# Kernel optimization log

Measured on AMD Instinct MI355X. Metric: run time of the kernel, lower is better.

The kernel has to match this reference:

```python
import jax, jax.numpy as jnp
import numpy as np

B, D = 90000, 100
E_GNN, E_MLP = 4, 4
E = E_GNN + E_MLP + 1  # 9
K = 2
NOISE_EPS = 0.01
LOSS_COEF = 0.4
GATE_MEAN, GATE_STD = 0.1, 1.0  # registered buffers in the torch module


def setup_inputs() -> dict:
    key = jax.random.key(0)
    ks = jax.random.split(key, 16)
    f = jax.random.normal
    return {
        "memory_feats": f(ks[0], (B, D), jnp.float32),
        "recent_raw": f(ks[1], (B, E_MLP, D), jnp.float32),
        "spatial_raw": f(ks[2], (B, E_GNN, D), jnp.float32),
        "node_feats_src": f(ks[3], (B, D), jnp.float32),
        "noise": f(ks[4], (B, E), jnp.float32),
        "deg_coef": f(ks[5], (1, D, 2), jnp.float32),
        "w_gate": f(ks[6], (6 * D, E), jnp.float32) * 0.05,
        "w_noise": f(ks[7], (6 * D, E), jnp.float32) * 0.05,
        "src_w": f(ks[8], (D, D), jnp.float32) * 0.1,
        "src_b": f(ks[9], (D,), jnp.float32) * 0.1,
        "dst_w": f(ks[10], (D, D), jnp.float32) * 0.1,
        "dst_b": f(ks[11], (D,), jnp.float32) * 0.1,
        "out_w": f(ks[12], (D, 1), jnp.float32) * 0.1,
        "out_b": f(ks[13], (1,), jnp.float32) * 0.1,
        "degree": jax.random.randint(ks[14], (B,), 0, 64, jnp.int32),
        "neg_samples": 1,
    }


def _cv_squared(x):
    # torch .var() is unbiased (ddof=1)
    return jnp.var(x, ddof=1) / (jnp.mean(x) ** 2 + 1e-10)


def _norm_cdf(v):
    return jax.scipy.stats.norm.cdf(v, loc=GATE_MEAN, scale=GATE_STD)


def reference(memory_feats, recent_raw, spatial_raw, node_feats_src, noise,
              deg_coef, w_gate, w_noise, src_w, src_b, dst_w, dst_b,
              out_w, out_b, degree, neg_samples):
    # memory expert output (dropout is identity in eval; relu applied)
    mem = jax.nn.relu(memory_feats)                        # [B, D]
    rec = jax.nn.relu(recent_raw)                          # [B, Em, D]
    log_deg = jnp.log(degree.astype(mem.dtype) + 1.0)      # [B]
    # degree-conditioned reweighting: stack([r, r*log_deg],-1) * deg_coef, sum(-1)
    c0, c1 = deg_coef[0, :, 0], deg_coef[0, :, 1]          # [D]
    spa = spatial_raw * (c0 + log_deg[:, None, None] * c1)  # [B, Eg, D]

    combine = jnp.concatenate([mem[:, None, :], spa, rec], axis=1)  # [B, E, D]
    result_spa = spa.mean(axis=1)
    result_rec = rec.mean(axis=1)
    x1 = mem + result_spa + result_rec
    x2 = mem * result_spa * result_rec
    cat = jnp.concatenate([mem, result_spa, result_rec, x1, x2, node_feats_src], axis=1)  # [B, 6D]

    # noisy top-k gating (train=True)
    clean = cat @ w_gate                                   # [B, E]
    std = jax.nn.softplus(cat @ w_noise) + NOISE_EPS
    noisy = clean + noise * std
    top_vals, top_idx = jax.lax.top_k(noisy, K + 1)        # [B, K+1]
    topk_gates = jax.nn.softmax(top_vals[:, :K], axis=1)
    b_idx = jnp.arange(noisy.shape[0])[:, None]
    gates = jnp.zeros_like(noisy).at[b_idx, top_idx[:, :K]].set(topk_gates)

    # prob of being in top-k for load-balance loss
    thr_in = top_vals[:, K][:, None]
    thr_out = top_vals[:, K - 1][:, None]
    is_in = noisy > thr_in
    prob = jnp.where(is_in,
                     _norm_cdf((clean - thr_in) / std),
                     _norm_cdf((clean - thr_out) / std))
    load = prob.sum(axis=0)
    importance = gates.sum(axis=0)
    loss = LOSS_COEF * (_cv_squared(importance) + _cv_squared(load))

    out = jnp.einsum('bed,be->bd', combine, gates)         # [B, D]

    # edge predictor
    num_edge = out.shape[0] // (neg_samples + 2)
    h_src = out[:num_edge] @ src_w + src_b
    h_pos = out[num_edge:2 * num_edge] @ dst_w + dst_b
    h_neg = out[2 * num_edge:] @ dst_w + dst_b
    pos = jax.nn.relu(h_src + h_pos) @ out_w + out_b       # [num_edge, 1]
    neg = jax.nn.relu(jnp.tile(h_src, (neg_samples, 1)) + h_neg) @ out_w + out_b
    return pos, neg, loss
```

## Files before the change

### kernel.cpp

```cpp
#include <hip/hip_runtime.h>
#include <math.h>

#define DD 100

#define DPP_ADD(v, ctrl) ((v) + __int_as_float(__builtin_amdgcn_update_dpp( \
    0, __float_as_int(v), (ctrl), 0xf, 0xf, true)))

__device__ __forceinline__ float blo(unsigned u){
  union { unsigned i; float f; } c; c.i = u << 16; return c.f;
}
__device__ __forceinline__ float bhi(unsigned u){
  union { unsigned i; float f; } c; c.i = u & 0xFFFF0000u; return c.f;
}
__device__ __forceinline__ unsigned short f2bf(float f){
  unsigned u = __float_as_uint(f);
  unsigned r = (u + 0x7FFFu + ((u >> 16) & 1u)) >> 16;
  return (unsigned short)r;
}
__device__ __forceinline__ float phi_fast(float z){
  float x  = z * 0.70710678118654752440f;
  float ax = fabsf(x);
  float t  = __builtin_amdgcn_rcpf(1.0f + 0.3275911f*ax);
  float p  = t*(0.254829592f + t*(-0.284496736f + t*(1.421413741f
           + t*(-1.453152027f + t*1.061405429f))));
  float e  = __expf(-ax*ax);
  float erfv = copysignf(1.0f - p*e, x);
  return 0.5f*(1.0f + erfv);
}
__device__ __forceinline__ float4 relu4(float4 v){
  return make_float4(fmaxf(v.x,0.f), fmaxf(v.y,0.f), fmaxf(v.z,0.f), fmaxf(v.w,0.f));
}
#define GETJ4(v,j) ((j==0)?(v).x:(j==1)?(v).y:(j==2)?(v).z:(v).w)

__global__ void k_fold(const float* __restrict__ wg, const float* __restrict__ wn,
                       float* __restrict__ wfold)
{
  int idx = blockIdx.x*256 + threadIdx.x;
  if (idx >= 9000) return;
  int dim = idx/90, r = idx%90, s = r/18, e = r%18;
  const float* W = (e < 9) ? wg : wn;
  int ee = (e < 9) ? e : e-9;
  int rowA = (s==0) ? dim : (s==1) ? 100+dim : (s==2) ? 200+dim
           : (s==3) ? 400+dim : 500+dim;
  float v = W[rowA*9 + ee] + ((s < 3) ? W[(300+dim)*9 + ee] : 0.f);
  wfold[idx] = v;
}

__global__ __launch_bounds__(256) void k_gate(
    const float* __restrict__ memf, const float* __restrict__ recr,
    const float* __restrict__ spar, const float* __restrict__ nsrc,
    const float* __restrict__ noise, const float* __restrict__ degc,
    const float* __restrict__ wfold, const int* __restrict__ degree,
    float4* __restrict__ gateinfo, float* __restrict__ partials, int B)
{
  __shared__ __align__(16) float sWF[100*92];
  __shared__ __align__(16) float sC0[DD], sC1[DD];
  __shared__ float sPart[4][18];

  for (int i = threadIdx.x; i < 9000; i += 256){
    int d = i/90, r = i%90;
    int slot = (d>>2) + 25*(d&3);
    sWF[slot*92 + r] = wfold[i];
  }
  for (int i = threadIdx.x; i < DD; i += 256){ sC0[i]=degc[2*i]; sC1[i]=degc[2*i+1]; }
  __syncthreads();

  const int wave = threadIdx.x >> 6, lane = threadIdx.x & 63;
  const int fq = lane & 3, rl = lane >> 2;
  const float4* sC04 = (const float4*)sC0;
  const float4* sC14 = (const float4*)sC1;

  float ldA[9], imA[9];
  #pragma unroll
  for (int e = 0; e < 9; e++){ ldA[e]=0.f; imA[e]=0.f; }

  const int rA = blockIdx.x*128 + wave*32 + rl*2;
  const int rB = rA + 1;
  const bool vA = rA < B, vB = rB < B;
  const int rcA = vA ? rA : B-1, rcB = vB ? rB : B-1;
  const float ldgA = __logf((float)degree[rcA] + 1.0f);
  const float ldgB = __logf((float)degree[rcB] + 1.0f);

  const float* pmA = memf + (size_t)rcA*DD;  const float* pmB = memf + (size_t)rcB*DD;
  const float* psA = spar + (size_t)rcA*4*DD;const float* psB = spar + (size_t)rcB*4*DD;
  const float* prA = recr + (size_t)rcA*4*DD;const float* prB = recr + (size_t)rcB*4*DD;
  const float* pnA = nsrc + (size_t)rcA*DD;  const float* pnB = nsrc + (size_t)rcB*DD;

  float cgA[9], cnA[9], cgB[9], cnB[9];
  #pragma unroll
  for (int e = 0; e < 9; e++){ cgA[e]=0.f; cnA[e]=0.f; cgB[e]=0.f; cnB[e]=0.f; }

  for (int k = 0; k < 7; k++){
    const int c = fq + 4*k;
    const float fz = (c < 25) ? 1.f : 0.f;
    const int ce = (c < 25) ? c : 0;
    const float4 c04 = sC04[ce], c14 = sC14[ce];

    float4 dA0, dA1, dA2, dA3, dA4;
    {
      float4 me = *(const float4*)(pmA + 4*ce);
      float4 s0 = *(const float4*)(psA + 0*DD + 4*ce);
      float4 s1 = *(const float4*)(psA + 1*DD + 4*ce);
      float4 s2 = *(const float4*)(psA + 2*DD + 4*ce);
      float4 s3 = *(const float4*)(psA + 3*DD + 4*ce);
      float4 r0 = *(const float4*)(prA + 0*DD + 4*ce);
      float4 r1 = *(const float4*)(prA + 1*DD + 4*ce);
      float4 r2 = *(const float4*)(prA + 2*DD + 4*ce);
      float4 r3 = *(const float4*)(prA + 3*DD + 4*ce);
      float4 nv = *(const float4*)(pnA + 4*ce);
      float4 m4 = relu4(me);
      float4 sc = make_float4(c04.x + ldgA*c14.x, c04.y + ldgA*c14.y,
                              c04.z + ldgA*c14.z, c04.w + ldgA*c14.w);
      float4 rs4 = make_float4((s0.x+s1.x+s2.x+s3.x)*0.25f*sc.x,
                               (s0.y+s1.y+s2.y+s3.y)*0.25f*sc.y,
                               (s0.z+s1.z+s2.z+s3.z)*0.25f*sc.z,
                               (s0.w+s1.w+s2.w+s3.w)*0.25f*sc.w);
      float4 a0 = relu4(r0), a1 = relu4(r1), a2 = relu4(r2), a3 = relu4(r3);
      float4 rr4 = make_float4((a0.x+a1.x+a2.x+a3.x)*0.25f,
                               (a0.y+a1.y+a2.y+a3.y)*0.25f,
                               (a0.z+a1.z+a2.z+a3.z)*0.25f,
                               (a0.w+a1.w+a2.w+a3.w)*0.25f);
      dA0 = make_float4(m4.x*fz, m4.y*fz, m4.z*fz, m4.w*fz);
      dA1 = make_float4(rs4.x*fz, rs4.y*fz, rs4.z*fz, rs4.w*fz);
      dA2 = make_float4(rr4.x*fz, rr4.y*fz, rr4.z*fz, rr4.w*fz);
      dA4 = make_float4(nv.x*fz, nv.y*fz, nv.z*fz, nv.w*fz);
      dA3 = make_float4(dA0.x*dA1.x*dA2.x, dA0.y*dA1.y*dA2.y,
                        dA0.z*dA1.z*dA2.z, dA0.w*dA1.w*dA2.w);
    }
    float4 dB0, dB1, dB2, dB3, dB4;
    {
      float4 me = *(const float4*)(pmB + 4*ce);
      float4 s0 = *(const float4*)(psB + 0*DD + 4*ce);
      float4 s1 = *(const float4*)(psB + 1*DD + 4*ce);
      float4 s2 = *(const float4*)(psB + 2*DD + 4*ce);
      float4 s3 = *(const float4*)(psB + 3*DD + 4*ce);
      float4 r0 = *(const float4*)(prB + 0*DD + 4*ce);
      float4 r1 = *(const float4*)(prB + 1*DD + 4*ce);
      float4 r2 = *(const float4*)(prB + 2*DD + 4*ce);
      float4 r3 = *(const float4*)(prB + 3*DD + 4*ce);
      float4 nv = *(const float4*)(pnB + 4*ce);
      float4 m4 = relu4(me);
      float4 sc = make_float4(c04.x + ldgB*c14.x, c04.y + ldgB*c14.y,
                              c04.z + ldgB*c14.z, c04.w + ldgB*c14.w);
      float4 rs4 = make_float4((s0.x+s1.x+s2.x+s3.x)*0.25f*sc.x,
                               (s0.y+s1.y+s2.y+s3.y)*0.25f*sc.y,
                               (s0.z+s1.z+s2.z+s3.z)*0.25f*sc.z,
                               (s0.w+s1.w+s2.w+s3.w)*0.25f*sc.w);
      float4 a0 = relu4(r0), a1 = relu4(r1), a2 = relu4(r2), a3 = relu4(r3);
      float4 rr4 = make_float4((a0.x+a1.x+a2.x+a3.x)*0.25f,
                               (a0.y+a1.y+a2.y+a3.y)*0.25f,
                               (a0.z+a1.z+a2.z+a3.z)*0.25f,
                               (a0.w+a1.w+a2.w+a3.w)*0.25f);
      dB0 = make_float4(m4.x*fz, m4.y*fz, m4.z*fz, m4.w*fz);
      dB1 = make_float4(rs4.x*fz, rs4.y*fz, rs4.z*fz, rs4.w*fz);
      dB2 = make_float4(rr4.x*fz, rr4.y*fz, rr4.z*fz, rr4.w*fz);
      dB4 = make_float4(nv.x*fz, nv.y*fz, nv.z*fz, nv.w*fz);
      dB3 = make_float4(dB0.x*dB1.x*dB2.x, dB0.y*dB1.y*dB2.y,
                        dB0.z*dB1.z*dB2.z, dB0.w*dB1.w*dB2.w);
    }

    #pragma unroll
    for (int j = 0; j < 4; j++){
      const float a0 = GETJ4(dA0,j), a1 = GETJ4(dA1,j), a2 = GETJ4(dA2,j);
      const float a3 = GETJ4(dA3,j), a4 = GETJ4(dA4,j);
      const float b0 = GETJ4(dB0,j), b1 = GETJ4(dB1,j), b2 = GETJ4(dB2,j);
      const float b3 = GETJ4(dB3,j), b4 = GETJ4(dB4,j);
      const float4* wpj = (const float4*)(sWF + (ce + 25*j)*92);
      #pragma unroll
      for (int tq = 0; tq < 23; tq++){
        float4 w = wpj[tq];
        #pragma unroll
        for (int u = 0; u < 4; u++){
          const int ww = 4*tq + u;
          if (ww < 90){
            const int seg = ww/18, e = ww%18;
            float wv = (u==0)?w.x:(u==1)?w.y:(u==2)?w.z:w.w;
            float dA = (seg==0)?a0:(seg==1)?a1:(seg==2)?a2:(seg==3)?a3:a4;
            float dB = (seg==0)?b0:(seg==1)?b1:(seg==2)?b2:(seg==3)?b3:b4;
            if (e < 9){ cgA[e] += dA*wv; cgB[e] += dB*wv; }
            else      { cnA[e-9] += dA*wv; cnB[e-9] += dB*wv; }
          }
        }
      }
    }
  }

  #pragma unroll
  for (int e = 0; e < 9; e++){
    cgA[e] = DPP_ADD(cgA[e], 0xB1); cgA[e] = DPP_ADD(cgA[e], 0x4E);
    cnA[e] = DPP_ADD(cnA[e], 0xB1); cnA[e] = DPP_ADD(cnA[e], 0x4E);
    cgB[e] = DPP_ADD(cgB[e], 0xB1); cgB[e] = DPP_ADD(cgB[e], 0x4E);
    cnB[e] = DPP_ADD(cnB[e], 0xB1); cnB[e] = DPP_ADD(cnB[e], 0x4E);
  }

  const bool selB = (fq >= 2);
  const int rowS = selB ? rB : rA;
  const bool vS = rowS < B;
  const int rcS = vS ? rowS : B-1;
  float fg[9], fn[9];
  #pragma unroll
  for (int e = 0; e < 9; e++){
    fg[e] = selB ? cgB[e] : cgA[e];
    fn[e] = selB ? cnB[e] : cnA[e];
  }

  float sdv[9], rsd[9], nz[9];
  #pragma unroll
  for (int e = 0; e < 9; e++){
    float x = fn[e];
    float spl = fmaxf(x, 0.f) + __logf(1.0f + __expf(-fabsf(x)));
    sdv[e] = spl + 0.01f;
    rsd[e] = __builtin_amdgcn_rcpf(sdv[e]);
    nz[e]  = fg[e] + noise[(size_t)rcS*9 + e] * sdv[e];
  }
  float v1 = -3.402823e38f, v2 = v1, v3 = v1; int i1 = -1, i2 = -1;
  #pragma unroll
  for (int e = 0; e < 9; e++){
    float v = nz[e];
    if (v > v1){ v3=v2; v2=v1; i2=i1; v1=v; i1=e; }
    else if (v > v2){ v3=v2; v2=v; i2=e; }
    else if (v > v3){ v3=v; }
  }
  float tt = __expf(v2 - v1);
  float g1 = __builtin_amdgcn_rcpf(1.0f + tt);
  float g2 = tt*g1;

  float ld[9], im[9];
  #pragma unroll
  for (int e = 0; e < 9; e++){
    float thr = (nz[e] > v3) ? v3 : v2;
    float z = (fg[e] - thr)*rsd[e] - 0.1f;
    ld[e] = vS ? phi_fast(z) : 0.f;
    im[e] = vS ? ((e==i1) ? g1 : ((e==i2) ? g2 : 0.f)) : 0.f;
  }
  if ((fq & 1) == 0 && vS)
    gateinfo[rowS] = make_float4(g1, g2, __int_as_float(i1), __int_as_float(i2));

  #pragma unroll
  for (int e = 0; e < 9; e++){
    #pragma unroll
    for (int off = 4; off < 64; off <<= 1){
      ld[e] += __shfl_xor(ld[e], off, 64);
      im[e] += __shfl_xor(im[e], off, 64);
    }
    ld[e] += __shfl_xor(ld[e], 2, 64);
    im[e] += __shfl_xor(im[e], 2, 64);
  }
  if (lane == 0){
    #pragma unroll
    for (int e = 0; e < 9; e++){ sPart[wave][e] = im[e]; sPart[wave][9+e] = ld[e]; }
  }
  __syncthreads();
  if (threadIdx.x < 18){
    float s = sPart[0][threadIdx.x] + sPart[1][threadIdx.x]
            + sPart[2][threadIdx.x] + sPart[3][threadIdx.x];
    partials[blockIdx.x*18 + threadIdx.x] = s;
  }
}

__global__ __launch_bounds__(256) void k_mix(
    const float* __restrict__ memf, const float* __restrict__ recr,
    const float* __restrict__ spar, const float* __restrict__ degc,
    const int* __restrict__ degree, const float4* __restrict__ gateinfo,
    float* __restrict__ outm, int B)
{
  const int total = B*25;
  for (int idx = blockIdx.x*256 + threadIdx.x; idx < total; idx += gridDim.x*256){
    int row = idx / 25, q = idx - row*25;
    float4 gi = gateinfo[row];
    float gv[2] = {gi.x, gi.y};
    int   ei[2] = {__float_as_int(gi.z), __float_as_int(gi.w)};
    float4 acc = make_float4(0.f,0.f,0.f,0.f);
    #pragma unroll
    for (int s = 0; s < 2; s++){
      int e = ei[s]; float g = gv[s];
      float4 v;
      if (e == 0){
        v = relu4(*(const float4*)(memf + (size_t)row*DD + 4*q));
      } else if (e < 5){
        float ldg = __logf((float)degree[row] + 1.0f);
        float4 ca = *(const float4*)(degc + 8*q);
        float4 cb = *(const float4*)(degc + 8*q + 4);
        float4 sv = *(const float4*)(spar + ((size_t)row*4 + (e-1))*DD + 4*q);
        v = make_float4(sv.x*(ca.x + ldg*ca.y), sv.y*(ca.z + ldg*ca.w),
                        sv.z*(cb.x + ldg*cb.y), sv.w*(cb.z + ldg*cb.w));
      } else {
        v = relu4(*(const float4*)(recr + ((size_t)row*4 + (e-5))*DD + 4*q));
      }
      acc.x += g*v.x; acc.y += g*v.y; acc.z += g*v.z; acc.w += g*v.w;
    }
    ((float4*)outm)[(size_t)row*25 + q] = acc;
  }
}

__global__ __launch_bounds__(1024) void k_loss(const float* __restrict__ partials,
                                               int nblk, float* __restrict__ dloss)
{
  __shared__ float sS[18][57];
  int t = threadIdx.x;
  if (t < 1008){
    int k = t % 18, c = t / 18;
    float s = 0.f;
    for (int b = c; b < nblk; b += 56) s += partials[b*18 + k];
    sS[k][c] = s;
  }
  __syncthreads();
  if (t < 18){
    float tot = 0.f;
    #pragma unroll
    for (int c = 0; c < 56; c++) tot += sS[t][c];
    sS[t][56] = tot;
  }
  __syncthreads();
  if (t == 0){
    float mi = 0.f, ml = 0.f;
    #pragma unroll
    for (int e = 0; e < 9; e++){ mi += sS[e][56]; ml += sS[9+e][56]; }
    mi *= (1.f/9.f); ml *= (1.f/9.f);
    float vi = 0.f, vl = 0.f;
    #pragma unroll
    for (int e = 0; e < 9; e++){
      float a = sS[e][56]   - mi; vi += a*a;
      float b = sS[9+e][56] - ml; vl += b*b;
    }
    vi *= (1.f/8.f); vl *= (1.f/8.f);
    *dloss = 0.4f * (vi/(mi*mi + 1e-10f) + vl/(ml*ml + 1e-10f));
  }
}

__global__ __launch_bounds__(512) void k_edge(
    const float* __restrict__ om,
    const float* __restrict__ sw, const float* __restrict__ sb,
    const float* __restrict__ dw, const float* __restrict__ db,
    const float* __restrict__ ow, const float* __restrict__ ob,
    float* __restrict__ dout, int NE)
{
  __shared__ __align__(4) unsigned short sSW[DD*102];
  __shared__ __align__(4) unsigned short sDW[DD*102];
  __shared__ float sSB[DD], sDB[DD], sOW[DD];

  for (int i = threadIdx.x; i < DD*DD; i += 512){
    int k = i / DD, d = i % DD;
    sSW[d*102 + k] = f2bf(sw[i]);
    sDW[d*102 + k] = f2bf(dw[i]);
  }
  for (int i = threadIdx.x; i < DD; i += 512){ sSB[i]=sb[i]; sDB[i]=db[i]; sOW[i]=ow[i]; }
  __syncthreads();

  const int wave = threadIdx.x >> 6, lane = threadIdx.x & 63;
  const int grp = blockIdx.x*8 + wave;
  const int e0 = grp*4;
  if (e0 >= NE) return;
  const int e0u = __builtin_amdgcn_readfirstlane(e0);
  const float* oS = om + (size_t)e0u*DD;
  const float* oP = om + ((size_t)(NE  + e0u))*DD;
  const float* oN = om + ((size_t)(2*NE + e0u))*DD;
  const int d0 = lane, d1 = lane + 64;
  const bool h1 = (d1 < DD);
  const int dc1 = h1 ? d1 : 0;

  float aS[4][2], aP[4][2], aN[4][2];
  #pragma unroll
  for (int r = 0; r < 4; r++){
    aS[r][0]=0.f; aS[r][1]=0.f; aP[r][0]=0.f; aP[r][1]=0.f; aN[r][0]=0.f; aN[r][1]=0.f;
  }

  for (int k = 0; k < DD; k += 4){
    unsigned uA = *(const unsigned*)&sSW[d0 *102 + k];
    unsigned uB = *(const unsigned*)&sSW[d0 *102 + k + 2];
    unsigned uC = *(const unsigned*)&sSW[dc1*102 + k];
    unsigned uD = *(const unsigned*)&sSW[dc1*102 + k + 2];
    unsigned uE = *(const unsigned*)&sDW[d0 *102 + k];
    unsigned uF = *(const unsigned*)&sDW[d0 *102 + k + 2];
    unsigned uG = *(const unsigned*)&sDW[dc1*102 + k];
    unsigned uH = *(const unsigned*)&sDW[dc1*102 + k + 2];
    float wS00=blo(uA), wS01=bhi(uA), wS02=blo(uB), wS03=bhi(uB);
    float wS10=blo(uC), wS11=bhi(uC), wS12=blo(uD), wS13=bhi(uD);
    float wD00=blo(uE), wD01=bhi(uE), wD02=blo(uF), wD03=bhi(uF);
    float wD10=blo(uG), wD11=bhi(uG), wD12=blo(uH), wD13=bhi(uH);
    #pragma unroll
    for (int r = 0; r < 4; r++){
      float4 ov = *(const float4*)(oS + r*DD + k);
      float4 pv = *(const float4*)(oP + r*DD + k);
      float4 nv = *(const float4*)(oN + r*DD + k);
      aS[r][0] += ov.x*wS00 + ov.y*wS01 + ov.z*wS02 + ov.w*wS03;
      aS[r][1] += ov.x*wS10 + ov.y*wS11 + ov.z*wS12 + ov.w*wS13;
      aP[r][0] += pv.x*wD00 + pv.y*wD01 + pv.z*wD02 + pv.w*wD03;
      aP[r][1] += pv.x*wD10 + pv.y*wD11 + pv.z*wD12 + pv.w*wD13;
      aN[r][0] += nv.x*wD00 + nv.y*wD01 + nv.z*wD02 + nv.w*wD03;
      aN[r][1] += nv.x*wD10 + nv.y*wD11 + nv.z*wD12 + nv.w*wD13;
    }
  }

  float owa = sOW[d0], owb = sOW[dc1];
  float sba = sSB[d0], sbb = sSB[dc1];
  float dba = sDB[d0], dbb = sDB[dc1];
  float ob0 = ob[0];
  #pragma unroll
  for (int r = 0; r < 4; r++){
    float hs0 = aS[r][0] + sba, hp0 = aP[r][0] + dba, hn0 = aN[r][0] + dba;
    float tp = fmaxf(hs0 + hp0, 0.f)*owa;
    float tn = fmaxf(hs0 + hn0, 0.f)*owa;
    if (h1){
      float hs1 = aS[r][1] + sbb, hp1 = aP[r][1] + dbb, hn1 = aN[r][1] + dbb;
      tp += fmaxf(hs1 + hp1, 0.f)*owb;
      tn += fmaxf(hs1 + hn1, 0.f)*owb;
    }
    #pragma unroll
    for (int off = 32; off > 0; off >>= 1){
      tp += __shfl_xor(tp, off, 64);
      tn += __shfl_xor(tn, off, 64);
    }
    if (lane == 0){
      dout[e0 + r]      = tp + ob0;
      dout[NE + e0 + r] = tn + ob0;
    }
  }
}

extern "C" void kernel_launch(void* const* d_in, const int* in_sizes, int n_in,
                              void* d_out, int out_size, void* d_ws, size_t ws_size,
                              hipStream_t stream)
{
  (void)n_in; (void)out_size; (void)ws_size;
  const float* memf  = (const float*)d_in[0];
  const float* recr  = (const float*)d_in[1];
  const float* spar  = (const float*)d_in[2];
  const float* nsrc  = (const float*)d_in[3];
  const float* noise = (const float*)d_in[4];
  const float* degc  = (const float*)d_in[5];
  const float* wg    = (const float*)d_in[6];
  const float* wn    = (const float*)d_in[7];
  const float* sw    = (const float*)d_in[8];
  const float* sb    = (const float*)d_in[9];
  const float* dw    = (const float*)d_in[10];
  const float* db    = (const float*)d_in[11];
  const float* ow    = (const float*)d_in[12];
  const float* ob    = (const float*)d_in[13];
  const int*   deg   = (const int*)d_in[14];

  const int B  = in_sizes[0] / DD;
  const int NE = B / 3;
  const int blocksA = (B + 127) / 128;

  float4* gateinfo = (float4*)d_ws;
  float*  outm     = (float*)(gateinfo + B);
  float*  partials = outm + (size_t)B*DD;
  float*  wfold    = partials + (size_t)blocksA*18;
  float*  dout     = (float*)d_out;

  k_fold<<<dim3(36), dim3(256), 0, stream>>>(wg, wn, wfold);
  k_gate<<<dim3(blocksA), dim3(256), 0, stream>>>(memf, recr, spar, nsrc, noise,
                                                  degc, wfold, deg, gateinfo,
                                                  partials, B);
  k_mix<<<dim3(2048), dim3(256), 0, stream>>>(memf, recr, spar, degc, deg,
                                              gateinfo, outm, B);
  k_loss<<<dim3(1), dim3(1024), 0, stream>>>(partials, blocksA, dout + 2*NE);
  const int blocks2 = (NE/4 + 7) / 8;
  k_edge<<<dim3(blocks2), dim3(512), 0, stream>>>(outm, sw, sb, dw, db, ow, ob, dout, NE);
}
```

Measured before the change: 264.5 us.

## Split gate GEMV work across lanes by dimension parity and gate/noise half

```diff
diff --git a/kernel.cpp b/kernel.cpp
--- a/kernel.cpp
+++ b/kernel.cpp
@@ -30,51 +30,41 @@
 __device__ __forceinline__ float4 relu4(float4 v){
   return make_float4(fmaxf(v.x,0.f), fmaxf(v.y,0.f), fmaxf(v.z,0.f), fmaxf(v.w,0.f));
 }
-#define GETJ4(v,j) ((j==0)?(v).x:(j==1)?(v).y:(j==2)?(v).z:(v).w)
 
 __global__ void k_fold(const float* __restrict__ wg, const float* __restrict__ wn,
-                       float* __restrict__ wfold)
+                       float* __restrict__ wfold2)
 {
   int idx = blockIdx.x*256 + threadIdx.x;
   if (idx >= 9000) return;
-  int dim = idx/90, r = idx%90, s = r/18, e = r%18;
-  const float* W = (e < 9) ? wg : wn;
-  int ee = (e < 9) ? e : e-9;
+  int dim = idx/90, r = idx%90, eh = r/45, i = r%45, s = i/9, e = i%9;
+  const float* W = eh ? wn : wg;
   int rowA = (s==0) ? dim : (s==1) ? 100+dim : (s==2) ? 200+dim
            : (s==3) ? 400+dim : 500+dim;
-  float v = W[rowA*9 + ee] + ((s < 3) ? W[(300+dim)*9 + ee] : 0.f);
-  wfold[idx] = v;
+  float v = W[rowA*9 + e] + ((s < 3) ? W[(300+dim)*9 + e] : 0.f);
+  wfold2[(dim*2 + eh)*52 + i] = v;
 }
 
 __global__ __launch_bounds__(256) void k_gate(
     const float* __restrict__ memf, const float* __restrict__ recr,
     const float* __restrict__ spar, const float* __restrict__ nsrc,
     const float* __restrict__ noise, const float* __restrict__ degc,
-    const float* __restrict__ wfold, const int* __restrict__ degree,
+    const float* __restrict__ wfold2, const int* __restrict__ degree,
     float4* __restrict__ gateinfo, float* __restrict__ partials, int B)
 {
-  __shared__ __align__(16) float sWF[100*92];
-  __shared__ __align__(16) float sC0[DD], sC1[DD];
+  __shared__ __align__(16) float sW2[200*52];
+  __shared__ __align__(8) float2 sCC[DD];
   __shared__ float sPart[4][18];
 
-  for (int i = threadIdx.x; i < 9000; i += 256){
-    int d = i/90, r = i%90;
-    int slot = (d>>2) + 25*(d&3);
-    sWF[slot*92 + r] = wfold[i];
-  }
-  for (int i = threadIdx.x; i < DD; i += 256){ sC0[i]=degc[2*i]; sC1[i]=degc[2*i+1]; }
+  for (int i = threadIdx.x; i < 10400; i += 256) sW2[i] = wfold2[i];
+  for (int i = threadIdx.x; i < DD; i += 256)
+    sCC[i] = make_float2(degc[2*i], degc[2*i+1]);
   __syncthreads();
 
   const int wave = threadIdx.x >> 6, lane = threadIdx.x & 63;
-  const int fq = lane & 3, rl = lane >> 2;
-  const float4* sC04 = (const float4*)sC0;
-  const float4* sC14 = (const float4*)sC1;
-
-  float ldA[9], imA[9];
-  #pragma unroll
-  for (int e = 0; e < 9; e++){ ldA[e]=0.f; imA[e]=0.f; }
-
-  const int rA = blockIdx.x*128 + wave*32 + rl*2;
+  const int fq = lane & 3, grp = lane >> 2;
+  const int dp = fq & 1, eh = fq >> 1;
+
+  const int rA = blockIdx.x*128 + wave*32 + grp*2;
   const int rB = rA + 1;
   const bool vA = rA < B, vB = rB < B;
   const int rcA = vA ? rA : B-1, rcB = vB ? rB : B-1;
@@ -86,111 +76,92 @@
   const float* prA = recr + (size_t)rcA*4*DD;const float* prB = recr + (size_t)rcB*4*DD;
   const float* pnA = nsrc + (size_t)rcA*DD;  const float* pnB = nsrc + (size_t)rcB*DD;
 
-  float cgA[9], cnA[9], cgB[9], cnB[9];
-  #pragma unroll
-  for (int e = 0; e < 9; e++){ cgA[e]=0.f; cnA[e]=0.f; cgB[e]=0.f; cnB[e]=0.f; }
-
-  for (int k = 0; k < 7; k++){
-    const int c = fq + 4*k;
-    const float fz = (c < 25) ? 1.f : 0.f;
-    const int ce = (c < 25) ? c : 0;
-    const float4 c04 = sC04[ce], c14 = sC14[ce];
-
-    float4 dA0, dA1, dA2, dA3, dA4;
+  float accA[9], accB[9];
+  #pragma unroll
+  for (int e = 0; e < 9; e++){ accA[e]=0.f; accB[e]=0.f; }
+
+  for (int k = 0; k < 50; k++){
+    const int d2 = 2*k;
+    const int dim = d2 + dp;
+    const float2 cc = sCC[dim];
+
+    float fA0, fA1, fA2, fA3, fA4;
     {
-      float4 me = *(const float4*)(pmA + 4*ce);
-      float4 s0 = *(const float4*)(psA + 0*DD + 4*ce);
-      float4 s1 = *(const float4*)(psA + 1*DD + 4*ce);
-      float4 s2 = *(const float4*)(psA + 2*DD + 4*ce);
-      float4 s3 = *(const float4*)(psA + 3*DD + 4*ce);
-      float4 r0 = *(const float4*)(prA + 0*DD + 4*ce);
-      float4 r1 = *(const float4*)(prA + 1*DD + 4*ce);
-      float4 r2 = *(const float4*)(prA + 2*DD + 4*ce);
-      float4 r3 = *(const float4*)(prA + 3*DD + 4*ce);
-      float4 nv = *(const float4*)(pnA + 4*ce);
-      float4 m4 = relu4(me);
-      float4 sc = make_float4(c04.x + ldgA*c14.x, c04.y + ldgA*c14.y,
-                              c04.z + ldgA*c14.z, c04.w + ldgA*c14.w);
-      float4 rs4 = make_float4((s0.x+s1.x+s2.x+s3.x)*0.25f*sc.x,
-                               (s0.y+s1.y+s2.y+s3.y)*0.25f*sc.y,
-                               (s0.z+s1.z+s2.z+s3.z)*0.25f*sc.z,
-                               (s0.w+s1.w+s2.w+s3.w)*0.25f*sc.w);
-      float4 a0 = relu4(r0), a1 = relu4(r1), a2 = relu4(r2), a3 = relu4(r3);
-      float4 rr4 = make_float4((a0.x+a1.x+a2.x+a3.x)*0.25f,
-                               (a0.y+a1.y+a2.y+a3.y)*0.25f,
-                               (a0.z+a1.z+a2.z+a3.z)*0.25f,
-                               (a0.w+a1.w+a2.w+a3.w)*0.25f);
-      dA0 = make_float4(m4.x*fz, m4.y*fz, m4.z*fz, m4.w*fz);
-      dA1 = make_float4(rs4.x*fz, rs4.y*fz, rs4.z*fz, rs4.w*fz);
-      dA2 = make_float4(rr4.x*fz, rr4.y*fz, rr4.z*fz, rr4.w*fz);
-      dA4 = make_float4(nv.x*fz, nv.y*fz, nv.z*fz, nv.w*fz);
-      dA3 = make_float4(dA0.x*dA1.x*dA2.x, dA0.y*dA1.y*dA2.y,
-                        dA0.z*dA1.z*dA2.z, dA0.w*dA1.w*dA2.w);
-    }
-    float4 dB0, dB1, dB2, dB3, dB4;
+      float2 me = *(const float2*)(pmA + d2);
+      float2 s0 = *(const float2*)(psA + 0*DD + d2);
+      float2 s1 = *(const float2*)(psA + 1*DD + d2);
+      float2 s2 = *(const float2*)(psA + 2*DD + d2);
+      float2 s3 = *(const float2*)(psA + 3*DD + d2);
+      float2 r0 = *(const float2*)(prA + 0*DD + d2);
+      float2 r1 = *(const float2*)(prA + 1*DD + d2);
+      float2 r2 = *(const float2*)(prA + 2*DD + d2);
+      float2 r3 = *(const float2*)(prA + 3*DD + d2);
+      float2 nv = *(const float2*)(pnA + d2);
+      float mm = fmaxf(dp ? me.y : me.x, 0.f);
+      float sa = (dp ? s0.y : s0.x) + (dp ? s1.y : s1.x)
+               + (dp ? s2.y : s2.x) + (dp ? s3.y : s3.x);
+      float rr = fmaxf(dp ? r0.y : r0.x, 0.f) + fmaxf(dp ? r1.y : r1.x, 0.f)
+               + fmaxf(dp ? r2.y : r2.x, 0.f) + fmaxf(dp ? r3.y : r3.x, 0.f);
+      fA0 = mm;
+      fA1 = sa*0.25f*(cc.x + ldgA*cc.y);
+      fA2 = rr*0.25f;
+      fA3 = fA0*fA1*fA2;
+      fA4 = dp ? nv.y : nv.x;
+    }
+    float fB0, fB1, fB2, fB3, fB4;
     {
-      float4 me = *(const float4*)(pmB + 4*ce);
-      float4 s0 = *(const float4*)(psB + 0*DD + 4*ce);
-      float4 s1 = *(const float4*)(psB + 1*DD + 4*ce);
-      float4 s2 = *(const float4*)(psB + 2*DD + 4*ce);
-      float4 s3 = *(const float4*)(psB + 3*DD + 4*ce);
-      float4 r0 = *(const float4*)(prB + 0*DD + 4*ce);
-      float4 r1 = *(const float4*)(prB + 1*DD + 4*ce);
-      float4 r2 = *(const float4*)(prB + 2*DD + 4*ce);
-      float4 r3 = *(const float4*)(prB + 3*DD + 4*ce);
-      float4 nv = *(const float4*)(pnB + 4*ce);
-      float4 m4 = relu4(me);
-      float4 sc = make_float4(c04.x + ldgB*c14.x, c04.y + ldgB*c14.y,
-                              c04.z + ldgB*c14.z, c04.w + ldgB*c14.w);
-      float4 rs4 = make_float4((s0.x+s1.x+s2.x+s3.x)*0.25f*sc.x,
-                               (s0.y+s1.y+s2.y+s3.y)*0.25f*sc.y,
-                               (s0.z+s1.z+s2.z+s3.z)*0.25f*sc.z,
-                               (s0.w+s1.w+s2.w+s3.w)*0.25f*sc.w);
-      float4 a0 = relu4(r0), a1 = relu4(r1), a2 = relu4(r2), a3 = relu4(r3);
-      float4 rr4 = make_float4((a0.x+a1.x+a2.x+a3.x)*0.25f,
-                               (a0.y+a1.y+a2.y+a3.y)*0.25f,
-                               (a0.z+a1.z+a2.z+a3.z)*0.25f,
-                               (a0.w+a1.w+a2.w+a3.w)*0.25f);
-      dB0 = make_float4(m4.x*fz, m4.y*fz, m4.z*fz, m4.w*fz);
-      dB1 = make_float4(rs4.x*fz, rs4.y*fz, rs4.z*fz, rs4.w*fz);
-      dB2 = make_float4(rr4.x*fz, rr4.y*fz, rr4.z*fz, rr4.w*fz);
-      dB4 = make_float4(nv.x*fz, nv.y*fz, nv.z*fz, nv.w*fz);
-      dB3 = make_float4(dB0.x*dB1.x*dB2.x, dB0.y*dB1.y*dB2.y,
-                        dB0.z*dB1.z*dB2.z, dB0.w*dB1.w*dB2.w);
-    }
-
-    #pragma unroll
-    for (int j = 0; j < 4; j++){
-      const float a0 = GETJ4(dA0,j), a1 = GETJ4(dA1,j), a2 = GETJ4(dA2,j);
-      const float a3 = GETJ4(dA3,j), a4 = GETJ4(dA4,j);
-      const float b0 = GETJ4(dB0,j), b1 = GETJ4(dB1,j), b2 = GETJ4(dB2,j);
-      const float b3 = GETJ4(dB3,j), b4 = GETJ4(dB4,j);
-      const float4* wpj = (const float4*)(sWF + (ce + 25*j)*92);
+      float2 me = *(const float2*)(pmB + d2);
+      float2 s0 = *(const float2*)(psB + 0*DD + d2);
+      float2 s1 = *(const float2*)(psB + 1*DD + d2);
+      float2 s2 = *(const float2*)(psB + 2*DD + d2);
+      float2 s3 = *(const float2*)(psB + 3*DD + d2);
+      float2 r0 = *(const float2*)(prB + 0*DD + d2);
+      float2 r1 = *(const float2*)(prB + 1*DD + d2);
+      float2 r2 = *(const float2*)(prB + 2*DD + d2);
+      float2 r3 = *(const float2*)(prB + 3*DD + d2);
+      float2 nv = *(const float2*)(pnB + d2);
+      float mm = fmaxf(dp ? me.y : me.x, 0.f);
+      float sa = (dp ? s0.y : s0.x) + (dp ? s1.y : s1.x)
+               + (dp ? s2.y : s2.x) + (dp ? s3.y : s3.x);
+      float rr = fmaxf(dp ? r0.y : r0.x, 0.f) + fmaxf(dp ? r1.y : r1.x, 0.f)
+               + fmaxf(dp ? r2.y : r2.x, 0.f) + fmaxf(dp ? r3.y : r3.x, 0.f);
+      fB0 = mm;
+      fB1 = sa*0.25f*(cc.x + ldgB*cc.y);
+      fB2 = rr*0.25f;
+      fB3 = fB0*fB1*fB2;
+      fB4 = dp ? nv.y : nv.x;
+    }
+
+    const float4* wp = (const float4*)(sW2 + (size_t)(dim*2 + eh)*52);
+    #pragma unroll
+    for (int tq = 0; tq < 12; tq++){
+      float4 w = wp[tq];
       #pragma unroll
-      for (int tq = 0; tq < 23; tq++){
-        float4 w = wpj[tq];
-        #pragma unroll
-        for (int u = 0; u < 4; u++){
-          const int ww = 4*tq + u;
-          if (ww < 90){
-            const int seg = ww/18, e = ww%18;
-            float wv = (u==0)?w.x:(u==1)?w.y:(u==2)?w.z:w.w;
-            float dA = (seg==0)?a0:(seg==1)?a1:(seg==2)?a2:(seg==3)?a3:a4;
-            float dB = (seg==0)?b0:(seg==1)?b1:(seg==2)?b2:(seg==3)?b3:b4;
-            if (e < 9){ cgA[e] += dA*wv; cgB[e] += dB*wv; }
-            else      { cnA[e-9] += dA*wv; cnB[e-9] += dB*wv; }
-          }
+      for (int u = 0; u < 4; u++){
+        const int i = 4*tq + u;
+        if (i < 45){
+          const int s = i/9, e = i%9;
+          float wv = (u==0)?w.x:(u==1)?w.y:(u==2)?w.z:w.w;
+          float dA = (s==0)?fA0:(s==1)?fA1:(s==2)?fA2:(s==3)?fA3:fA4;
+          float dB = (s==0)?fB0:(s==1)?fB1:(s==2)?fB2:(s==3)?fB3:fB4;
+          accA[e] += dA*wv;
+          accB[e] += dB*wv;
         }
       }
     }
   }
 
-  #pragma unroll
-  for (int e = 0; e < 9; e++){
-    cgA[e] = DPP_ADD(cgA[e], 0xB1); cgA[e] = DPP_ADD(cgA[e], 0x4E);
-    cnA[e] = DPP_ADD(cnA[e], 0xB1); cnA[e] = DPP_ADD(cnA[e], 0x4E);
-    cgB[e] = DPP_ADD(cgB[e], 0xB1); cgB[e] = DPP_ADD(cgB[e], 0x4E);
-    cnB[e] = DPP_ADD(cnB[e], 0xB1); cnB[e] = DPP_ADD(cnB[e], 0x4E);
+  float cgA[9], cnA[9], cgB[9], cnB[9];
+  #pragma unroll
+  for (int e = 0; e < 9; e++){
+    float sA = DPP_ADD(accA[e], 0xB1);
+    float oA = __shfl_xor(sA, 2, 64);
+    cgA[e] = eh ? oA : sA;
+    cnA[e] = eh ? sA : oA;
+    float sB = DPP_ADD(accB[e], 0xB1);
+    float oB = __shfl_xor(sB, 2, 64);
+    cgB[e] = eh ? oB : sB;
+    cnB[e] = eh ? sB : oB;
   }
 
   const bool selB = (fq >= 2);
@@ -446,12 +417,12 @@
   float4* gateinfo = (float4*)d_ws;
   float*  outm     = (float*)(gateinfo + B);
   float*  partials = outm + (size_t)B*DD;
-  float*  wfold    = partials + (size_t)blocksA*18;
+  float*  wfold2   = partials + (size_t)blocksA*18;
   float*  dout     = (float*)d_out;
 
-  k_fold<<<dim3(36), dim3(256), 0, stream>>>(wg, wn, wfold);
+  k_fold<<<dim3(36), dim3(256), 0, stream>>>(wg, wn, wfold2);
   k_gate<<<dim3(blocksA), dim3(256), 0, stream>>>(memf, recr, spar, nsrc, noise,
-                                                  degc, wfold, deg, gateinfo,
+                                                  degc, wfold2, deg, gateinfo,
                                                   partials, B);
   k_mix<<<dim3(2048), dim3(256), 0, stream>>>(memf, recr, spar, degc, deg,
                                               gateinfo, outm, B);
```

After: 779.6 us. 2.95x slower.
